# Kernel tuning notes

Hardware: AMD Instinct MI355X
Metric: run time of the kernel (lower is better)

## Reference

```python
import jax, jax.numpy as jnp
import numpy as np
from math import factorial, sqrt

MUL = 128
BATCH = 16384
IRREPS_IN1 = [(MUL, 0, 1), (MUL, 1, -1), (MUL, 2, 1)]   # (mul, l, parity)
IRREPS_IN2 = [(1, 0, 1), (1, 1, -1), (1, 2, 1), (1, 3, -1)]
TARGET = {(0, 1), (1, -1), (2, 1), (3, -1)}               # allowed output (l, parity)


def _su2_cg(j1, m1, j2, m2, j3, m3):
    """Complex Clebsch-Gordan coefficient <j1 m1 j2 m2 | j3 m3> (Racah formula)."""
    if m1 + m2 != m3:
        return 0.0
    f = lambda n: float(factorial(n))
    pref = sqrt((2 * j3 + 1) * f(j1 + j2 - j3) * f(j1 - j2 + j3) * f(-j1 + j2 + j3) / f(j1 + j2 + j3 + 1))
    pref *= sqrt(f(j1 + m1) * f(j1 - m1) * f(j2 + m2) * f(j2 - m2) * f(j3 + m3) * f(j3 - m3))
    s = 0.0
    lo = max(0, j2 - j3 - m1, j1 - j3 + m2)
    hi = min(j1 + j2 - j3, j1 - m1, j2 + m2)
    for k in range(lo, hi + 1):
        s += (-1.0) ** k / (f(k) * f(j1 + j2 - j3 - k) * f(j1 - m1 - k) * f(j2 + m2 - k) * f(j3 - j2 + m1 + k) * f(j3 - j1 - m2 + k))
    return pref * s


def _q(l):
    """Change of basis real SH <- complex SH (e3nn convention, phased)."""
    q = np.zeros((2 * l + 1, 2 * l + 1), dtype=np.complex128)
    for m in range(-l, 0):
        q[l + m, l + abs(m)] = 1.0 / np.sqrt(2)
        q[l + m, l - abs(m)] = -1j / np.sqrt(2)
    q[l, l] = 1.0
    for m in range(1, l + 1):
        q[l + m, l + abs(m)] = (-1) ** m / np.sqrt(2)
        q[l + m, l - abs(m)] = 1j * (-1) ** m / np.sqrt(2)
    return (-1j) ** l * q


def _real_cg(l1, l2, l3):
    """Real-basis CG tensor [2l1+1, 2l2+1, 2l3+1], unit Frobenius norm."""
    Cc = np.zeros((2 * l1 + 1, 2 * l2 + 1, 2 * l3 + 1), dtype=np.complex128)
    for a, m1 in enumerate(range(-l1, l1 + 1)):
        for b, m2 in enumerate(range(-l2, l2 + 1)):
            for c, m3 in enumerate(range(-l3, l3 + 1)):
                Cc[a, b, c] = _su2_cg(l1, m1, l2, m2, l3, m3)
    C = np.einsum('abc,ia,jb,kc->ijk', Cc, np.conj(_q(l1)), np.conj(_q(l2)), _q(l3))
    re, im = np.real(C), np.imag(C)
    C = re if np.linalg.norm(re) >= np.linalg.norm(im) else im  # result is real up to a global phase
    return (C / np.linalg.norm(C)).astype(np.float32)


# enumerate channelwise ('uvu', mul2 == 1) paths allowed by CG selection rules + TARGET filter
PATHS = []
for i, (m1, l1, p1) in enumerate(IRREPS_IN1):
    for j, (m2, l2, p2) in enumerate(IRREPS_IN2):
        for l3 in range(abs(l1 - l2), l1 + l2 + 1):
            if (l3, p1 * p2) in TARGET:
                PATHS.append((i, j, l3))
ORDER = sorted(range(len(PATHS)), key=lambda k: PATHS[k][2])  # stable sort by output l
CG = {(IRREPS_IN1[i][1], IRREPS_IN2[j][1], l3): _real_cg(IRREPS_IN1[i][1], IRREPS_IN2[j][1], l3)
      for (i, j, l3) in PATHS}

OFF1 = np.cumsum([0] + [m * (2 * l + 1) for m, l, _ in IRREPS_IN1])
OFF2 = np.cumsum([0] + [m * (2 * l + 1) for m, l, _ in IRREPS_IN2])
DIM1, DIM2 = int(OFF1[-1]), int(OFF2[-1])          # 1152, 16
WEIGHT_NUMEL = MUL * len(PATHS)                     # 17 * 128 = 2176
DIM_OUT = sum(MUL * (2 * PATHS[k][2] + 1) for k in ORDER)  # 9088


def setup_inputs() -> dict:
    key = jax.random.key(0)
    k1, k2, k3 = jax.random.split(key, 3)
    return {
        'x1': jax.random.normal(k1, (BATCH, DIM1), dtype=jnp.float32),
        'x2': jax.random.normal(k2, (BATCH, DIM2), dtype=jnp.float32),
        'weights': jax.random.normal(k3, (BATCH, WEIGHT_NUMEL), dtype=jnp.float32),
    }


def reference(x1, x2, weights):
    B = x1.shape[0]
    # split mul_ir inputs into per-irrep segments
    x1s = [x1[:, int(OFF1[i]):int(OFF1[i + 1])].reshape(B, m, 2 * l + 1)
           for i, (m, l, _) in enumerate(IRREPS_IN1)]
    x2s = [x2[:, int(OFF2[j]):int(OFF2[j + 1])] for j in range(len(IRREPS_IN2))]  # mul2 == 1
    outs = []
    for k in ORDER:
        i, j, l3 = PATHS[k]
        l1, l2 = IRREPS_IN1[i][1], IRREPS_IN2[j][1]
        C = jnp.asarray(CG[(l1, l2, l3)])                  # [2l1+1, 2l2+1, 2l3+1]
        w = weights[:, k * MUL:(k + 1) * MUL]              # [B, mul] per-edge per-channel weights
        alpha = sqrt((2 * l3 + 1) / MUL)                   # component/element path normalization
        y = jnp.einsum('ijk,bui,bj->buk', C, x1s[i], x2s[j])  # [B, mul, 2l3+1]
        outs.append((alpha * w[:, :, None] * y).reshape(B, MUL * (2 * l3 + 1)))
    return jnp.concatenate(outs, axis=1)  # mul_ir layout, one slot per path, sorted by output l
```

## Files before the change

### kernel.cpp

```cpp
#include <hip/hip_runtime.h>


#define NPATH 17

namespace cgc {

constexpr double FT[16] = {1.,1.,2.,6.,24.,120.,720.,5040.,40320.,362880.,
  3628800.,39916800.,479001600.,6227020800.,87178291200.,1307674368000.};

constexpr double csqrt(double x){
  if (x <= 0.0) return 0.0;
  double g = x > 1.0 ? x : 1.0;
  for (int i=0;i<48;++i) g = 0.5*(g + x/g);
  return g;
}

constexpr double su2cg(int j1,int m1,int j2,int m2,int j3,int m3){
  if (m1+m2 != m3) return 0.0;
  double pref = csqrt((double)(2*j3+1)*FT[j1+j2-j3]*FT[j1-j2+j3]*FT[-j1+j2+j3]/FT[j1+j2+j3+1]);
  pref *= csqrt(FT[j1+m1]*FT[j1-m1]*FT[j2+m2]*FT[j2-m2]*FT[j3+m3]*FT[j3-m3]);
  int lo=0; if (j2-j3-m1>lo) lo=j2-j3-m1; if (j1-j3+m2>lo) lo=j1-j3+m2;
  int hi=j1+j2-j3; if (j1-m1<hi) hi=j1-m1; if (j2+m2<hi) hi=j2+m2;
  double s=0.0;
  for (int k=lo;k<=hi;++k){
    double d = FT[k]*FT[j1+j2-j3-k]*FT[j1-m1-k]*FT[j2+m2-k]*FT[j3-j2+m1+k]*FT[j3-j1-m2+k];
    s += ((k&1)? -1.0:1.0)/d;
  }
  return pref*s;
}

constexpr int qrow(int l, int r, int* cols, double* vr, double* vi){
  const double is2 = 0.70710678118654752440;
  int mp = r - l;
  int n = 0;
  double tr[2]={0,0}, ti[2]={0,0};
  if (mp < 0){ cols[0]=l-mp; tr[0]=is2; ti[0]=0.0; cols[1]=l+mp; tr[1]=0.0; ti[1]=-is2; n=2; }
  else if (mp==0){ cols[0]=l; tr[0]=1.0; ti[0]=0.0; n=1; }
  else { double sg=(mp&1)?-1.0:1.0; cols[0]=l+mp; tr[0]=sg*is2; ti[0]=0.0;
         cols[1]=l-mp; tr[1]=0.0; ti[1]=sg*is2; n=2; }
  int ph = l & 3;
  for (int t=0;t<n;++t){
    double re=tr[t], im=ti[t], nr=0, ni=0;
    if (ph==0){ nr=re; ni=im; } else if (ph==1){ nr=im; ni=-re; }
    else if (ph==2){ nr=-re; ni=-im; } else { nr=-im; ni=re; }
    vr[t]=nr; vi[t]=ni;
  }
  return n;
}

constexpr int PL1[NPATH] = {0,0,0,0, 1,1,1,1,1,1, 2,2,2,2,2,2,2};
constexpr int PL2[NPATH] = {0,1,2,3, 0,1,1,2,2,3, 0,1,1,2,2,3,3};
constexpr int PL3[NPATH] = {0,1,2,3, 1,0,2,1,3,2, 2,1,3,0,2,1,3};
constexpr int CGOFF[NPATH] = {0,1,10,35,84,93,102,147,192,297,402,427,472,577,602,727,832};
constexpr int X2OFF[NPATH] = {0,1,4,9, 0,1,1,4,4,9, 0,1,1,4,4,9,9};
constexpr int KOFF[NPATH]  = {0,4,8,16,24,36,40,56,68,92,108,136,152,188,196,224,240};
constexpr int KN[NPATH]    = {1,3,5,7, 9,3,15,9,21,15, 25,15,35,5,25,15,35};

struct CGTab { float v[1077]; };

constexpr CGTab make_cg(){
  CGTab R{};
  for (int p=0;p<NPATH;++p){
    const int l1=PL1[p], l2=PL2[p], l3=PL3[p];
    const int N1=2*l1+1, N2=2*l2+1, N3=2*l3+1;
    double cc[245] = {};
    for (int a=0;a<N1;++a) for (int b=0;b<N2;++b){
      int m1=a-l1, m2=b-l2, m3=m1+m2;
      if (m3>=-l3 && m3<=l3)
        cc[(a*N2+b)*N3 + (m3+l3)] = su2cg(l1,m1,l2,m2,l3,m3);
    }
    double re[245]={}, im[245]={};
    for (int i=0;i<N1;++i){
      int ca[2]={}; double ar[2]={}, ai[2]={};
      const int na=qrow(l1,i,ca,ar,ai);
      for (int j=0;j<N2;++j){
        int cb[2]={}; double br[2]={}, bi[2]={};
        const int nb=qrow(l2,j,cb,br,bi);
        for (int k=0;k<N3;++k){
          int cd[2]={}; double dr[2]={}, di[2]={};
          const int nd=qrow(l3,k,cd,dr,di);
          double sr=0, si=0;
          for (int x=0;x<na;++x) for (int y=0;y<nb;++y){
            const double r1=ar[x], i1=-ai[x];
            const double r2=br[y], i2=-bi[y];
            const double r12 = r1*r2 - i1*i2;
            const double i12 = r1*i2 + i1*r2;
            for (int z=0;z<nd;++z){
              const double cg = cc[(ca[x]*N2+cb[y])*N3 + cd[z]];
              if (cg != 0.0){
                sr += cg*(r12*dr[z] - i12*di[z]);
                si += cg*(r12*di[z] + i12*dr[z]);
              }
            }
          }
          re[(i*N2+j)*N3+k]=sr; im[(i*N2+j)*N3+k]=si;
        }
      }
    }
    const int n = N1*N2*N3;
    double nr=0, ni=0;
    for (int e=0;e<n;++e){ nr += re[e]*re[e]; ni += im[e]*im[e]; }
    const bool usere = (nr >= ni);
    const double sc = 1.0 / csqrt(usere ? nr : ni);
    for (int e=0;e<n;++e)
      R.v[CGOFF[p]+e] = (float)((usere ? re[e] : im[e]) * sc);
  }
  return R;
}

struct EMap { unsigned short cgbase, dst; unsigned char stride, cnt, x2off, pad; };
struct EMaps { EMap m[243]; };
constexpr EMaps make_emaps(){
  EMaps M{};
  int e=0;
  for (int p=0;p<NPATH;++p){
    const int l2=PL2[p], l3=PL3[p];
    const int N2=2*l2+1, N3=2*l3+1;
    for (int rem=0; rem<KN[p]; ++rem, ++e){
      const int i = rem / N3, k = rem % N3;
      M.m[e].cgbase = (unsigned short)(CGOFF[p] + i*N2*N3 + k);
      M.m[e].dst    = (unsigned short)(KOFF[p] + rem);
      M.m[e].stride = (unsigned char)N3;
      M.m[e].cnt    = (unsigned char)N2;
      M.m[e].x2off  = (unsigned char)X2OFF[p];
      M.m[e].pad    = 0;
    }
  }
  return M;
}

}

__device__ __constant__ cgc::CGTab c_cg  = cgc::make_cg();
__device__ __constant__ cgc::EMaps c_map = cgc::make_emaps();


template<int L1, int L3>
__device__ __forceinline__ void path_out(const float* __restrict__ Kp,
                                         const float* __restrict__ xv,
                                         float wa, float* __restrict__ op){
  constexpr int N1 = 2*L1+1, N3 = 2*L3+1;
  float y[N3];
#pragma unroll
  for (int k=0;k<N3;++k) y[k] = 0.0f;
#pragma unroll
  for (int i=0;i<N1;++i){
    const float a = xv[i];
#pragma unroll
    for (int k=0;k<N3;++k) y[k] = fmaf(Kp[i*N3+k], a, y[k]);
  }
#pragma unroll
  for (int k=0;k<N3;++k) op[k] = wa*y[k];
}

__global__ __launch_bounds__(256) void tp_main(const float* __restrict__ x1,
                                               const float* __restrict__ x2,
                                               const float* __restrict__ wts,
                                               float* __restrict__ out){
  __shared__ float sK[276];
  __shared__ __align__(16) float sOut[9088];
  const int tid = threadIdx.x;
  const int t   = tid >> 7;
  const int u   = tid & 127;
  const long long b = blockIdx.x;

  if (tid < 243){
    const cgc::EMap m = c_map.m[tid];
    const float* __restrict__ C  = c_cg.v + m.cgbase;
    const float* __restrict__ xx = x2 + b*16 + m.x2off;
    float acc = 0.f;
    for (int j=0;j<m.cnt;++j) acc = fmaf(C[j*m.stride], xx[j], acc);
    sK[m.dst] = acc;
  }
  __syncthreads();

  {
    const float* __restrict__ x1b = x1 + b*1152;
    const float* __restrict__ wb  = wts + b*2176 + u;
    const float* __restrict__ K   = sK;

    const float A0=0.08838834764831845f, A1=0.15309310892394863f,
                A2=0.19764235376052372f, A3=0.23385358667337133f;

    if (t == 0){
      float xa[4];
      xa[0] = x1b[u];
#pragma unroll
      for (int q=0;q<3;++q) xa[1+q] = x1b[128 + 3*u + q];
      float xc[5];
#pragma unroll
      for (int q=0;q<5;++q) xc[q] = x1b[512 + 5*u + q];
      path_out<0,0>(K+0,   xa,   wb[0*128]*A0,  sOut + 0    + u);
      path_out<0,1>(K+4,   xa,   wb[1*128]*A1,  sOut + 384  + u*3);
      path_out<0,2>(K+8,   xa,   wb[2*128]*A2,  sOut + 2304 + u*5);
      path_out<0,3>(K+16,  xa,   wb[3*128]*A3,  sOut + 5504 + u*7);
      path_out<1,1>(K+24,  xa+1, wb[4*128]*A1,  sOut + 768  + u*3);
      path_out<1,0>(K+36,  xa+1, wb[5*128]*A0,  sOut + 128  + u);
      path_out<1,2>(K+40,  xa+1, wb[6*128]*A2,  sOut + 2944 + u*5);
      path_out<1,1>(K+56,  xa+1, wb[7*128]*A1,  sOut + 1152 + u*3);
      path_out<1,3>(K+68,  xa+1, wb[8*128]*A3,  sOut + 6400 + u*7);
      path_out<1,2>(K+92,  xa+1, wb[9*128]*A2,  sOut + 3584 + u*5);
      path_out<2,0>(K+188, xc,   wb[13*128]*A0, sOut + 256  + u);
      path_out<2,2>(K+196, xc,   wb[14*128]*A2, sOut + 4864 + u*5);
    } else {
      float xc[5];
#pragma unroll
      for (int q=0;q<5;++q) xc[q] = x1b[512 + 5*u + q];
      path_out<2,2>(K+108, xc, wb[10*128]*A2, sOut + 4224 + u*5);
      path_out<2,1>(K+136, xc, wb[11*128]*A1, sOut + 1536 + u*3);
      path_out<2,3>(K+152, xc, wb[12*128]*A3, sOut + 7296 + u*7);
      path_out<2,1>(K+224, xc, wb[15*128]*A1, sOut + 1920 + u*3);
      path_out<2,3>(K+240, xc, wb[16*128]*A3, sOut + 8192 + u*7);
    }
  }
  __syncthreads();

  {
    float4* __restrict__ dst = (float4*)(out + b*9088);
    const float4* __restrict__ src = (const float4*)sOut;
    for (int idx = tid; idx < 2272; idx += 256)
      dst[idx] = src[idx];
  }
}


extern "C" void kernel_launch(void* const* d_in, const int* in_sizes, int n_in,
                              void* d_out, int out_size, void* d_ws, size_t ws_size,
                              hipStream_t stream) {
  const float* x1 = (const float*)d_in[0];
  const float* x2 = (const float*)d_in[1];
  const float* w  = (const float*)d_in[2];
  float* out = (float*)d_out;
  (void)d_ws; (void)ws_size; (void)in_sizes; (void)n_in; (void)out_size;

  tp_main<<<dim3(16384), dim3(256), 0, stream>>>(x1, x2, w, out);
}
```

Before: 167.2 us.

## Split output staging into two phases to shrink shared memory and rebalance paths

```diff
diff --git a/kernel.cpp b/kernel.cpp
--- a/kernel.cpp
+++ b/kernel.cpp
@@ -158,7 +158,7 @@
                                                const float* __restrict__ wts,
                                                float* __restrict__ out){
   __shared__ float sK[276];
-  __shared__ __align__(16) float sOut[9088];
+  __shared__ __align__(16) float sBuf[5504];
   const int tid = threadIdx.x;
   const int t   = tid >> 7;
   const int u   = tid & 127;
@@ -172,53 +172,64 @@
     for (int j=0;j<m.cnt;++j) acc = fmaf(C[j*m.stride], xx[j], acc);
     sK[m.dst] = acc;
   }
-  __syncthreads();
-
-  {
-    const float* __restrict__ x1b = x1 + b*1152;
-    const float* __restrict__ wb  = wts + b*2176 + u;
-    const float* __restrict__ K   = sK;
-
-    const float A0=0.08838834764831845f, A1=0.15309310892394863f,
-                A2=0.19764235376052372f, A3=0.23385358667337133f;
-
-    if (t == 0){
-      float xa[4];
-      xa[0] = x1b[u];
-#pragma unroll
-      for (int q=0;q<3;++q) xa[1+q] = x1b[128 + 3*u + q];
-      float xc[5];
-#pragma unroll
-      for (int q=0;q<5;++q) xc[q] = x1b[512 + 5*u + q];
-      path_out<0,0>(K+0,   xa,   wb[0*128]*A0,  sOut + 0    + u);
-      path_out<0,1>(K+4,   xa,   wb[1*128]*A1,  sOut + 384  + u*3);
-      path_out<0,2>(K+8,   xa,   wb[2*128]*A2,  sOut + 2304 + u*5);
-      path_out<0,3>(K+16,  xa,   wb[3*128]*A3,  sOut + 5504 + u*7);
-      path_out<1,1>(K+24,  xa+1, wb[4*128]*A1,  sOut + 768  + u*3);
-      path_out<1,0>(K+36,  xa+1, wb[5*128]*A0,  sOut + 128  + u);
-      path_out<1,2>(K+40,  xa+1, wb[6*128]*A2,  sOut + 2944 + u*5);
-      path_out<1,1>(K+56,  xa+1, wb[7*128]*A1,  sOut + 1152 + u*3);
-      path_out<1,3>(K+68,  xa+1, wb[8*128]*A3,  sOut + 6400 + u*7);
-      path_out<1,2>(K+92,  xa+1, wb[9*128]*A2,  sOut + 3584 + u*5);
-      path_out<2,0>(K+188, xc,   wb[13*128]*A0, sOut + 256  + u);
-      path_out<2,2>(K+196, xc,   wb[14*128]*A2, sOut + 4864 + u*5);
-    } else {
-      float xc[5];
-#pragma unroll
-      for (int q=0;q<5;++q) xc[q] = x1b[512 + 5*u + q];
-      path_out<2,2>(K+108, xc, wb[10*128]*A2, sOut + 4224 + u*5);
-      path_out<2,1>(K+136, xc, wb[11*128]*A1, sOut + 1536 + u*3);
-      path_out<2,3>(K+152, xc, wb[12*128]*A3, sOut + 7296 + u*7);
-      path_out<2,1>(K+224, xc, wb[15*128]*A1, sOut + 1920 + u*3);
-      path_out<2,3>(K+240, xc, wb[16*128]*A3, sOut + 8192 + u*7);
-    }
+
+  const float* __restrict__ x1b = x1 + b*1152;
+  float xa[4];
+  xa[0] = x1b[u];
+  float xc[5];
+#pragma unroll
+  for (int q=0;q<5;++q) xc[q] = x1b[512 + 5*u + q];
+  if (t == 0){
+#pragma unroll
+    for (int q=0;q<3;++q) xa[1+q] = x1b[128 + 3*u + q];
+  }
+
+  const float* __restrict__ wb = wts + b*2176 + u;
+  const float* __restrict__ K  = sK;
+  const float A0=0.08838834764831845f, A1=0.15309310892394863f,
+              A2=0.19764235376052372f, A3=0.23385358667337133f;
+
+  __syncthreads();
+
+  if (t == 0){
+    path_out<0,0>(K+0,   xa,   wb[0*128]*A0,  sBuf + 0    + u);
+    path_out<0,1>(K+4,   xa,   wb[1*128]*A1,  sBuf + 384  + u*3);
+    path_out<0,2>(K+8,   xa,   wb[2*128]*A2,  sBuf + 2304 + u*5);
+    path_out<1,1>(K+24,  xa+1, wb[4*128]*A1,  sBuf + 768  + u*3);
+    path_out<1,0>(K+36,  xa+1, wb[5*128]*A0,  sBuf + 128  + u);
+    path_out<1,2>(K+40,  xa+1, wb[6*128]*A2,  sBuf + 2944 + u*5);
+    path_out<1,1>(K+56,  xa+1, wb[7*128]*A1,  sBuf + 1152 + u*3);
+    path_out<1,2>(K+92,  xa+1, wb[9*128]*A2,  sBuf + 3584 + u*5);
+    path_out<2,1>(K+136, xc,   wb[11*128]*A1, sBuf + 1536 + u*3);
+  } else {
+    path_out<2,2>(K+108, xc, wb[10*128]*A2, sBuf + 4224 + u*5);
+    path_out<2,0>(K+188, xc, wb[13*128]*A0, sBuf + 256  + u);
+    path_out<2,2>(K+196, xc, wb[14*128]*A2, sBuf + 4864 + u*5);
+    path_out<2,1>(K+224, xc, wb[15*128]*A1, sBuf + 1920 + u*3);
   }
   __syncthreads();
 
   {
     float4* __restrict__ dst = (float4*)(out + b*9088);
-    const float4* __restrict__ src = (const float4*)sOut;
-    for (int idx = tid; idx < 2272; idx += 256)
+    const float4* __restrict__ src = (const float4*)sBuf;
+    for (int idx = tid; idx < 1376; idx += 256)
+      dst[idx] = src[idx];
+  }
+  __syncthreads();
+
+  if (t == 0){
+    path_out<1,3>(K+68,  xa+1, wb[8*128]*A3,  sBuf + 896  + u*7);
+    path_out<2,3>(K+152, xc,   wb[12*128]*A3, sBuf + 1792 + u*7);
+  } else {
+    path_out<0,3>(K+16,  xa, wb[3*128]*A3,  sBuf + 0    + u*7);
+    path_out<2,3>(K+240, xc, wb[16*128]*A3, sBuf + 2688 + u*7);
+  }
+  __syncthreads();
+
+  {
+    float4* __restrict__ dst = (float4*)(out + b*9088 + 5504);
+    const float4* __restrict__ src = (const float4*)sBuf;
+    for (int idx = tid; idx < 896; idx += 256)
       dst[idx] = src[idx];
   }
 }
```

New measurement: 170.7 us. +2.1%, slower.

## Compute output float4 chunks directly, removing shared-memory staging buffer

Applied to the files above, without the earlier changes.

```diff
diff --git a/kernel.cpp b/kernel.cpp
--- a/kernel.cpp
+++ b/kernel.cpp
@@ -135,22 +135,51 @@
 __device__ __constant__ cgc::EMaps c_map = cgc::make_emaps();
 
 
-template<int L1, int L3>
-__device__ __forceinline__ void path_out(const float* __restrict__ Kp,
-                                         const float* __restrict__ xv,
-                                         float wa, float* __restrict__ op){
-  constexpr int N1 = 2*L1+1, N3 = 2*L3+1;
-  float y[N3];
-#pragma unroll
-  for (int k=0;k<N3;++k) y[k] = 0.0f;
-#pragma unroll
-  for (int i=0;i<N1;++i){
-    const float a = xv[i];
-#pragma unroll
-    for (int k=0;k<N3;++k) y[k] = fmaf(Kp[i*N3+k], a, y[k]);
-  }
-#pragma unroll
-  for (int k=0;k<N3;++k) op[k] = wa*y[k];
+template<int N1, int KO>
+__device__ __forceinline__ float4 chunk_n3_1(int fo, const float* __restrict__ x1f,
+                                             const float* __restrict__ wcol, float alpha,
+                                             const float* __restrict__ K){
+  float kv[N1];
+#pragma unroll
+  for (int i=0;i<N1;++i) kv[i] = K[KO+i];
+  float4 o; float* op = (float*)&o;
+#pragma unroll
+  for (int t=0;t<4;++t){
+    const int u = fo + t;
+    float y = 0.f;
+#pragma unroll
+    for (int i=0;i<N1;++i) y = fmaf(kv[i], x1f[u*N1+i], y);
+    op[t] = alpha * wcol[u] * y;
+  }
+  return o;
+}
+
+template<int N1, int N3, int KO>
+__device__ __forceinline__ float4 chunk_gen(int fo, const float* __restrict__ x1f,
+                                            const float* __restrict__ wcol, float alpha,
+                                            const float* __restrict__ K){
+  const int u0 = fo / N3;
+  const int k0 = fo - u0*N3;
+  const int u1 = (k0 + 3 >= N3) ? u0 + 1 : u0;
+  const float w0 = alpha * wcol[u0];
+  const float w1 = alpha * wcol[u1];
+  float xa[N1], xb[N1];
+#pragma unroll
+  for (int i=0;i<N1;++i) xa[i] = x1f[u0*N1+i];
+#pragma unroll
+  for (int i=0;i<N1;++i) xb[i] = x1f[u1*N1+i];
+  float4 o; float* op = (float*)&o;
+#pragma unroll
+  for (int t=0;t<4;++t){
+    const int k = k0 + t;
+    const bool c = (k >= N3);
+    const int kk = c ? k - N3 : k;
+    float y = 0.f;
+#pragma unroll
+    for (int i=0;i<N1;++i) y = fmaf(K[KO + i*N3 + kk], c ? xb[i] : xa[i], y);
+    op[t] = (c ? w1 : w0) * y;
+  }
+  return o;
 }
 
 __global__ __launch_bounds__(256) void tp_main(const float* __restrict__ x1,
@@ -158,10 +187,7 @@
                                                const float* __restrict__ wts,
                                                float* __restrict__ out){
   __shared__ float sK[276];
-  __shared__ __align__(16) float sOut[9088];
   const int tid = threadIdx.x;
-  const int t   = tid >> 7;
-  const int u   = tid & 127;
   const long long b = blockIdx.x;
 
   if (tid < 243){
@@ -174,52 +200,50 @@
   }
   __syncthreads();
 
-  {
-    const float* __restrict__ x1b = x1 + b*1152;
-    const float* __restrict__ wb  = wts + b*2176 + u;
-    const float* __restrict__ K   = sK;
-
-    const float A0=0.08838834764831845f, A1=0.15309310892394863f,
-                A2=0.19764235376052372f, A3=0.23385358667337133f;
-
-    if (t == 0){
-      float xa[4];
-      xa[0] = x1b[u];
-#pragma unroll
-      for (int q=0;q<3;++q) xa[1+q] = x1b[128 + 3*u + q];
-      float xc[5];
-#pragma unroll
-      for (int q=0;q<5;++q) xc[q] = x1b[512 + 5*u + q];
-      path_out<0,0>(K+0,   xa,   wb[0*128]*A0,  sOut + 0    + u);
-      path_out<0,1>(K+4,   xa,   wb[1*128]*A1,  sOut + 384  + u*3);
-      path_out<0,2>(K+8,   xa,   wb[2*128]*A2,  sOut + 2304 + u*5);
-      path_out<0,3>(K+16,  xa,   wb[3*128]*A3,  sOut + 5504 + u*7);
-      path_out<1,1>(K+24,  xa+1, wb[4*128]*A1,  sOut + 768  + u*3);
-      path_out<1,0>(K+36,  xa+1, wb[5*128]*A0,  sOut + 128  + u);
-      path_out<1,2>(K+40,  xa+1, wb[6*128]*A2,  sOut + 2944 + u*5);
-      path_out<1,1>(K+56,  xa+1, wb[7*128]*A1,  sOut + 1152 + u*3);
-      path_out<1,3>(K+68,  xa+1, wb[8*128]*A3,  sOut + 6400 + u*7);
-      path_out<1,2>(K+92,  xa+1, wb[9*128]*A2,  sOut + 3584 + u*5);
-      path_out<2,0>(K+188, xc,   wb[13*128]*A0, sOut + 256  + u);
-      path_out<2,2>(K+196, xc,   wb[14*128]*A2, sOut + 4864 + u*5);
+  const float* __restrict__ x1b = x1 + b*1152;
+  const float* __restrict__ wb  = wts + b*2176;
+  const float* __restrict__ K   = sK;
+  float4* __restrict__ orow     = (float4*)(out + b*9088);
+
+  const float A0=0.08838834764831845f, A1=0.15309310892394863f,
+              A2=0.19764235376052372f, A3=0.23385358667337133f;
+
+#pragma unroll 1
+  for (int v = tid; v < 2272; v += 256){
+    float4 res;
+    if (v < 96){
+      const int blk = v >> 5, fo = (v & 31)*4;
+      if      (blk == 0) res = chunk_n3_1<1,0  >(fo, x1b+0,   wb+0*128,  A0, K);
+      else if (blk == 1) res = chunk_n3_1<3,36 >(fo, x1b+128, wb+5*128,  A0, K);
+      else               res = chunk_n3_1<5,188>(fo, x1b+512, wb+13*128, A0, K);
+    } else if (v < 576){
+      const int vv = v - 96, blk = vv/96, fo = (vv - blk*96)*4;
+      switch (blk){
+        case 0:  res = chunk_gen<1,3,4  >(fo, x1b+0,   wb+1*128,  A1, K); break;
+        case 1:  res = chunk_gen<3,3,24 >(fo, x1b+128, wb+4*128,  A1, K); break;
+        case 2:  res = chunk_gen<3,3,56 >(fo, x1b+128, wb+7*128,  A1, K); break;
+        case 3:  res = chunk_gen<5,3,136>(fo, x1b+512, wb+11*128, A1, K); break;
+        default: res = chunk_gen<5,3,224>(fo, x1b+512, wb+15*128, A1, K); break;
+      }
+    } else if (v < 1376){
+      const int vv = v - 576, blk = vv/160, fo = (vv - blk*160)*4;
+      switch (blk){
+        case 0:  res = chunk_gen<1,5,8  >(fo, x1b+0,   wb+2*128,  A2, K); break;
+        case 1:  res = chunk_gen<3,5,40 >(fo, x1b+128, wb+6*128,  A2, K); break;
+        case 2:  res = chunk_gen<3,5,92 >(fo, x1b+128, wb+9*128,  A2, K); break;
+        case 3:  res = chunk_gen<5,5,108>(fo, x1b+512, wb+10*128, A2, K); break;
+        default: res = chunk_gen<5,5,196>(fo, x1b+512, wb+14*128, A2, K); break;
+      }
     } else {
-      float xc[5];
-#pragma unroll
-      for (int q=0;q<5;++q) xc[q] = x1b[512 + 5*u + q];
-      path_out<2,2>(K+108, xc, wb[10*128]*A2, sOut + 4224 + u*5);
-      path_out<2,1>(K+136, xc, wb[11*128]*A1, sOut + 1536 + u*3);
-      path_out<2,3>(K+152, xc, wb[12*128]*A3, sOut + 7296 + u*7);
-      path_out<2,1>(K+224, xc, wb[15*128]*A1, sOut + 1920 + u*3);
-      path_out<2,3>(K+240, xc, wb[16*128]*A3, sOut + 8192 + u*7);
-    }
-  }
-  __syncthreads();
-
-  {
-    float4* __restrict__ dst = (float4*)(out + b*9088);
-    const float4* __restrict__ src = (const float4*)sOut;
-    for (int idx = tid; idx < 2272; idx += 256)
-      dst[idx] = src[idx];
+      const int vv = v - 1376, blk = vv/224, fo = (vv - blk*224)*4;
+      switch (blk){
+        case 0:  res = chunk_gen<1,7,16 >(fo, x1b+0,   wb+3*128,  A3, K); break;
+        case 1:  res = chunk_gen<3,7,68 >(fo, x1b+128, wb+8*128,  A3, K); break;
+        case 2:  res = chunk_gen<5,7,152>(fo, x1b+512, wb+12*128, A3, K); break;
+        default: res = chunk_gen<5,7,240>(fo, x1b+512, wb+16*128, A3, K); break;
+      }
+    }
+    orow[v] = res;
   }
 }
 
```

New measurement: 259.8 us. 1.55x slower.

## Make each wavefront independent with per-wave CG kernels and staged stores

Applied to the files above, without the earlier changes.

```diff
diff --git a/kernel.cpp b/kernel.cpp
--- a/kernel.cpp
+++ b/kernel.cpp
@@ -55,6 +55,10 @@
 constexpr int X2OFF[NPATH] = {0,1,4,9, 0,1,1,4,4,9, 0,1,1,4,4,9,9};
 constexpr int KOFF[NPATH]  = {0,4,8,16,24,36,40,56,68,92,108,136,152,188,196,224,240};
 constexpr int KN[NPATH]    = {1,3,5,7, 9,3,15,9,21,15, 25,15,35,5,25,15,35};
+constexpr int OUTB[NPATH]  = {0,384,2304,5504, 768,128,2944,1152,6400,3584,
+                              4224,1536,7296,256,4864,1920,8192};
+constexpr float ALPH[4] = {0.08838834764831845f, 0.15309310892394863f,
+                           0.19764235376052372f, 0.23385358667337133f};
 
 struct CGTab { float v[1077]; };
 
@@ -135,91 +139,117 @@
 __device__ __constant__ cgc::EMaps c_map = cgc::make_emaps();
 
 
-template<int L1, int L3>
-__device__ __forceinline__ void path_out(const float* __restrict__ Kp,
-                                         const float* __restrict__ xv,
-                                         float wa, float* __restrict__ op){
+template<int P>
+__device__ __forceinline__ void do_path(const int h, const int lane,
+    const float* __restrict__ x1b, const float* __restrict__ wrow,
+    const float* __restrict__ Kw, float* __restrict__ stage,
+    float* __restrict__ outrow){
+  constexpr int L1 = cgc::PL1[P], L3 = cgc::PL3[P];
   constexpr int N1 = 2*L1+1, N3 = 2*L3+1;
+  constexpr int KO = cgc::KOFF[P];
+  constexpr int X1O = (L1==0) ? 0 : (L1==1 ? 128 : 512);
+  constexpr int OB = cgc::OUTB[P];
+  constexpr float AL = cgc::ALPH[L3];
+
+  const int u = h*64 + lane;
+  float x[N1];
+#pragma unroll
+  for (int i=0;i<N1;++i) x[i] = x1b[X1O + u*N1 + i];
+  const float wv = AL * wrow[P*128 + u];
   float y[N3];
 #pragma unroll
-  for (int k=0;k<N3;++k) y[k] = 0.0f;
-#pragma unroll
-  for (int i=0;i<N1;++i){
-    const float a = xv[i];
-#pragma unroll
-    for (int k=0;k<N3;++k) y[k] = fmaf(Kp[i*N3+k], a, y[k]);
-  }
-#pragma unroll
-  for (int k=0;k<N3;++k) op[k] = wa*y[k];
+  for (int k=0;k<N3;++k) y[k] = 0.f;
+#pragma unroll
+  for (int i=0;i<N1;++i)
+#pragma unroll
+    for (int k=0;k<N3;++k) y[k] = fmaf(Kw[KO + i*N3 + k], x[i], y[k]);
+#pragma unroll
+  for (int k=0;k<N3;++k) stage[lane*N3 + k] = wv*y[k];
+  asm volatile("s_waitcnt lgkmcnt(0)" ::: "memory");
+  constexpr int NF4 = 16*N3;
+  float4* __restrict__ dst = (float4*)(outrow + OB + h*(64*N3));
+  const float4* __restrict__ src = (const float4*)stage;
+  if constexpr (NF4 <= 64){
+    if (lane < NF4) dst[lane] = src[lane];
+  } else {
+    dst[lane] = src[lane];
+    if (lane < NF4-64) dst[64+lane] = src[64+lane];
+  }
 }
 
 __global__ __launch_bounds__(256) void tp_main(const float* __restrict__ x1,
                                                const float* __restrict__ x2,
                                                const float* __restrict__ wts,
                                                float* __restrict__ out){
-  __shared__ float sK[276];
-  __shared__ __align__(16) float sOut[9088];
-  const int tid = threadIdx.x;
-  const int t   = tid >> 7;
-  const int u   = tid & 127;
+  __shared__ __align__(16) float sK[4*280];
+  __shared__ __align__(16) float sStage[4*2*448];
+  const int tid  = threadIdx.x;
+  const int wid  = tid >> 6;
+  const int lane = tid & 63;
   const long long b = blockIdx.x;
 
-  if (tid < 243){
-    const cgc::EMap m = c_map.m[tid];
-    const float* __restrict__ C  = c_cg.v + m.cgbase;
-    const float* __restrict__ xx = x2 + b*16 + m.x2off;
-    float acc = 0.f;
-    for (int j=0;j<m.cnt;++j) acc = fmaf(C[j*m.stride], xx[j], acc);
-    sK[m.dst] = acc;
-  }
-  __syncthreads();
-
+  const float* __restrict__ x1b  = x1  + b*1152;
+  const float* __restrict__ x2b  = x2  + b*16;
+  const float* __restrict__ wrow = wts + b*2176;
+  float* __restrict__ outrow     = out + b*9088;
+
+  float* __restrict__ Kw = sK + wid*280;
   {
-    const float* __restrict__ x1b = x1 + b*1152;
-    const float* __restrict__ wb  = wts + b*2176 + u;
-    const float* __restrict__ K   = sK;
-
-    const float A0=0.08838834764831845f, A1=0.15309310892394863f,
-                A2=0.19764235376052372f, A3=0.23385358667337133f;
-
-    if (t == 0){
-      float xa[4];
-      xa[0] = x1b[u];
-#pragma unroll
-      for (int q=0;q<3;++q) xa[1+q] = x1b[128 + 3*u + q];
-      float xc[5];
-#pragma unroll
-      for (int q=0;q<5;++q) xc[q] = x1b[512 + 5*u + q];
-      path_out<0,0>(K+0,   xa,   wb[0*128]*A0,  sOut + 0    + u);
-      path_out<0,1>(K+4,   xa,   wb[1*128]*A1,  sOut + 384  + u*3);
-      path_out<0,2>(K+8,   xa,   wb[2*128]*A2,  sOut + 2304 + u*5);
-      path_out<0,3>(K+16,  xa,   wb[3*128]*A3,  sOut + 5504 + u*7);
-      path_out<1,1>(K+24,  xa+1, wb[4*128]*A1,  sOut + 768  + u*3);
-      path_out<1,0>(K+36,  xa+1, wb[5*128]*A0,  sOut + 128  + u);
-      path_out<1,2>(K+40,  xa+1, wb[6*128]*A2,  sOut + 2944 + u*5);
-      path_out<1,1>(K+56,  xa+1, wb[7*128]*A1,  sOut + 1152 + u*3);
-      path_out<1,3>(K+68,  xa+1, wb[8*128]*A3,  sOut + 6400 + u*7);
-      path_out<1,2>(K+92,  xa+1, wb[9*128]*A2,  sOut + 3584 + u*5);
-      path_out<2,0>(K+188, xc,   wb[13*128]*A0, sOut + 256  + u);
-      path_out<2,2>(K+196, xc,   wb[14*128]*A2, sOut + 4864 + u*5);
-    } else {
-      float xc[5];
-#pragma unroll
-      for (int q=0;q<5;++q) xc[q] = x1b[512 + 5*u + q];
-      path_out<2,2>(K+108, xc, wb[10*128]*A2, sOut + 4224 + u*5);
-      path_out<2,1>(K+136, xc, wb[11*128]*A1, sOut + 1536 + u*3);
-      path_out<2,3>(K+152, xc, wb[12*128]*A3, sOut + 7296 + u*7);
-      path_out<2,1>(K+224, xc, wb[15*128]*A1, sOut + 1920 + u*3);
-      path_out<2,3>(K+240, xc, wb[16*128]*A3, sOut + 8192 + u*7);
-    }
-  }
-  __syncthreads();
-
-  {
-    float4* __restrict__ dst = (float4*)(out + b*9088);
-    const float4* __restrict__ src = (const float4*)sOut;
-    for (int idx = tid; idx < 2272; idx += 256)
-      dst[idx] = src[idx];
+#pragma unroll
+    for (int r=0;r<4;++r){
+      const int e = lane + r*64;
+      if (e < 243){
+        const cgc::EMap m = c_map.m[e];
+        const float* __restrict__ C = c_cg.v + m.cgbase;
+        float acc = 0.f;
+        for (int j=0;j<m.cnt;++j) acc = fmaf(C[j*m.stride], x2b[m.x2off + j], acc);
+        Kw[m.dst] = acc;
+      }
+    }
+  }
+  asm volatile("s_waitcnt lgkmcnt(0)" ::: "memory");
+
+  float* __restrict__ st0 = sStage + wid*896;
+  float* __restrict__ st1 = st0 + 448;
+
+  if (wid == 0){
+    do_path<12>(0, lane, x1b, wrow, Kw, st0, outrow);
+    do_path<12>(1, lane, x1b, wrow, Kw, st1, outrow);
+    do_path<10>(0, lane, x1b, wrow, Kw, st0, outrow);
+    do_path< 8>(0, lane, x1b, wrow, Kw, st1, outrow);
+    do_path<13>(0, lane, x1b, wrow, Kw, st0, outrow);
+  } else if (wid == 1){
+    do_path<16>(0, lane, x1b, wrow, Kw, st0, outrow);
+    do_path<16>(1, lane, x1b, wrow, Kw, st1, outrow);
+    do_path<10>(1, lane, x1b, wrow, Kw, st0, outrow);
+    do_path< 8>(1, lane, x1b, wrow, Kw, st1, outrow);
+    do_path<13>(1, lane, x1b, wrow, Kw, st0, outrow);
+  } else if (wid == 2){
+    do_path<14>(0, lane, x1b, wrow, Kw, st0, outrow);
+    do_path<14>(1, lane, x1b, wrow, Kw, st1, outrow);
+    do_path< 6>(0, lane, x1b, wrow, Kw, st0, outrow);
+    do_path< 6>(1, lane, x1b, wrow, Kw, st1, outrow);
+    do_path< 9>(0, lane, x1b, wrow, Kw, st0, outrow);
+    do_path< 9>(1, lane, x1b, wrow, Kw, st1, outrow);
+    do_path< 4>(0, lane, x1b, wrow, Kw, st0, outrow);
+    do_path< 2>(0, lane, x1b, wrow, Kw, st1, outrow);
+    do_path< 1>(0, lane, x1b, wrow, Kw, st0, outrow);
+    do_path< 0>(0, lane, x1b, wrow, Kw, st1, outrow);
+  } else {
+    do_path<11>(0, lane, x1b, wrow, Kw, st0, outrow);
+    do_path<11>(1, lane, x1b, wrow, Kw, st1, outrow);
+    do_path<15>(0, lane, x1b, wrow, Kw, st0, outrow);
+    do_path<15>(1, lane, x1b, wrow, Kw, st1, outrow);
+    do_path< 7>(0, lane, x1b, wrow, Kw, st0, outrow);
+    do_path< 7>(1, lane, x1b, wrow, Kw, st1, outrow);
+    do_path< 4>(1, lane, x1b, wrow, Kw, st0, outrow);
+    do_path< 3>(0, lane, x1b, wrow, Kw, st1, outrow);
+    do_path< 3>(1, lane, x1b, wrow, Kw, st0, outrow);
+    do_path< 2>(1, lane, x1b, wrow, Kw, st1, outrow);
+    do_path< 5>(0, lane, x1b, wrow, Kw, st0, outrow);
+    do_path< 5>(1, lane, x1b, wrow, Kw, st1, outrow);
+    do_path< 1>(1, lane, x1b, wrow, Kw, st0, outrow);
+    do_path< 0>(1, lane, x1b, wrow, Kw, st1, outrow);
   }
 }
 
```

Result: slower. 276.4 us (+65.4%).
